# Performance work log

Hardware: AMD Instinct MI355X
Metric: run time of the kernel (lower is better)

The kernel has to match this reference:

```python
import jax, jax.numpy as jnp
import numpy as np

B, S, D, H = 2, 2048, 1024, 16
DK = D // H


def setup_inputs() -> dict:
    key = jax.random.key(0)
    ks = jax.random.split(key, 12)
    q = jax.random.normal(ks[0], (B, S, D), dtype=jnp.float32)
    k = jax.random.normal(ks[1], (B, S, D), dtype=jnp.float32)
    v = jax.random.normal(ks[2], (B, S, D), dtype=jnp.float32)
    # causal mask: 1 = attend, 0 = masked (masked_fill(mask==0, -inf))
    mask = jnp.tril(jnp.ones((S, S), dtype=jnp.int32))[None, None]
    w = 0.02
    Wq = jax.random.normal(ks[3], (D, D), dtype=jnp.float32) * w
    bq = jnp.zeros((D,), dtype=jnp.float32)
    Wk = jax.random.normal(ks[4], (D, D), dtype=jnp.float32) * w
    bk = jnp.zeros((D,), dtype=jnp.float32)
    Wv = jax.random.normal(ks[5], (D, D), dtype=jnp.float32) * w
    bv = jnp.zeros((D,), dtype=jnp.float32)
    Wo = jax.random.normal(ks[6], (D, D), dtype=jnp.float32) * w
    bo = jnp.zeros((D,), dtype=jnp.float32)
    return {"q": q, "k": k, "v": v, "mask": mask,
            "Wq": Wq, "bq": bq, "Wk": Wk, "bk": bk,
            "Wv": Wv, "bv": bv, "Wo": Wo, "bo": bo}


def _split_heads(x):
    b, s, _ = x.shape
    return x.reshape(b, s, H, DK).transpose(0, 2, 1, 3)  # [B,H,S,DK]


def reference(q, k, v, mask, Wq, bq, Wk, bk, Wv, bv, Wo, bo):
    qh = _split_heads(q @ Wq.T + bq)
    kh = _split_heads(k @ Wk.T + bk)
    vh = _split_heads(v @ Wv.T + bv)
    scale = 1.0 / jnp.sqrt(jnp.float32(DK))
    scores = jnp.einsum("bhqd,bhkd->bhqk", qh, kh) * scale  # [B,H,S,S]
    scores = jnp.where(mask == 0, -jnp.inf, scores)
    pesos = jax.nn.softmax(scores, axis=-1)
    pesos = jnp.nan_to_num(pesos, nan=0.0)  # fully-masked rows -> 0
    out = jnp.einsum("bhqk,bhkd->bhqd", pesos, vh)
    out = out.transpose(0, 2, 1, 3).reshape(q.shape[0], q.shape[1], D)
    # dropout is identity at inference
    return out @ Wo.T + bo
```

## Files before the change

kernel.cpp:

```cpp
#include <hip/hip_runtime.h>
#include <hip/hip_bf16.h>

#define B_  2
#define S_  2048
#define D_  1024
#define H_  16
#define DK_ 64

using bf16 = __hip_bfloat16;
typedef __bf16 bf16x8 __attribute__((ext_vector_type(8)));
typedef float  f32x4  __attribute__((ext_vector_type(4)));

__device__ inline void st1(float* p, float v) { *p = v; }
__device__ inline void st1(bf16*  p, float v) { *p = __float2bfloat16(v); }

__device__ inline void gll16(const bf16* g, bf16* l) {
    __builtin_amdgcn_global_load_lds(
        (const __attribute__((address_space(1))) unsigned int*)g,
        (__attribute__((address_space(3))) unsigned int*)l, 16, 0, 0);
}

__global__ __launch_bounds__(256) void cvt_kernel(
    const float* __restrict__ s0, const float* __restrict__ s1,
    const float* __restrict__ s2, const float* __restrict__ s3,
    const float* __restrict__ s4, const float* __restrict__ s5,
    const float* __restrict__ s6,
    bf16* __restrict__ d0, bf16* __restrict__ d1, bf16* __restrict__ d2,
    bf16* __restrict__ d3, bf16* __restrict__ d4, bf16* __restrict__ d5,
    bf16* __restrict__ d6, int nbig, int nsmall)
{
    const int z = blockIdx.y;
    const float* s; bf16* d; int n;
    switch (z) {
        case 0: s = s0; d = d0; n = nbig;   break;
        case 1: s = s1; d = d1; n = nbig;   break;
        case 2: s = s2; d = d2; n = nbig;   break;
        case 3: s = s3; d = d3; n = nsmall; break;
        case 4: s = s4; d = d4; n = nsmall; break;
        case 5: s = s5; d = d5; n = nsmall; break;
        default: s = s6; d = d6; n = nsmall; break;
    }
    const int idx = (blockIdx.x * 256 + threadIdx.x) * 4;
    if (idx < n) {
        const float4 v = *reinterpret_cast<const float4*>(s + idx);
        union { ushort4 u; __bf16 h[4]; } r;
        r.h[0] = (__bf16)v.x; r.h[1] = (__bf16)v.y;
        r.h[2] = (__bf16)v.z; r.h[3] = (__bf16)v.w;
        *reinterpret_cast<ushort4*>(d + idx) = r.u;
    }
}

template <typename TC, bool VT3, int BM>
__global__ __launch_bounds__(256, BM == 128 ? 3 : 4) void gemm_bt_kernel(
    const bf16* __restrict__ A0, const bf16* __restrict__ A1, const bf16* __restrict__ A2,
    const bf16* __restrict__ W0, const bf16* __restrict__ W1, const bf16* __restrict__ W2,
    const float* __restrict__ b0, const float* __restrict__ b1, const float* __restrict__ b2,
    TC* __restrict__ C0, TC* __restrict__ C1, TC* __restrict__ C2,
    int M, int N, int K)
{
    const int z = blockIdx.z;
    const bf16*  A    = (z == 0) ? A0 : (z == 1) ? A1 : A2;
    const bf16*  W    = (z == 0) ? W0 : (z == 1) ? W1 : W2;
    const float* bias = (z == 0) ? b0 : (z == 1) ? b1 : b2;
    TC*          C    = (z == 0) ? C0 : (z == 1) ? C1 : C2;

    __shared__ bf16 As[BM][32];
    __shared__ bf16 Bs[128][32];

    const int t    = threadIdx.x;
    const int lane = t & 63;
    const int wave = t >> 6;
    const int quad = lane >> 4;
    const int l16  = lane & 15;
    const int wm   = wave >> 1;
    const int wn   = wave & 1;

    const int m0 = blockIdx.y * BM;
    const int n0 = blockIdx.x * 128;

    constexpr int RPW = BM / 4;
    constexpr int MI  = BM / 32;
    const int ar0 = wave * RPW + (lane >> 2);
    const int br0 = wave * 32  + (lane >> 2);
    const int c0  = (lane & 3) * 8;
    const bf16* Ab = A + (size_t)(m0 + ar0) * K + c0;
    const bf16* Bb = W + (size_t)(n0 + br0) * K + c0;
    bf16* asd = &As[wave * RPW][0];
    bf16* bsd = &Bs[wave * 32][0];

    f32x4 acc[MI][4] = {};

    for (int kt = 0; kt < K; kt += 32) {
        __syncthreads();
        gll16(Ab + kt, asd);
        if constexpr (BM == 128) gll16(Ab + 16 * K + kt, asd + 16 * 32);
        gll16(Bb + kt, bsd);
        gll16(Bb + 16 * K + kt, bsd + 16 * 32);
        __syncthreads();

        bf16x8 af[MI], bfr[4];
#pragma unroll
        for (int mi = 0; mi < MI; mi++)
            af[mi] = *reinterpret_cast<const bf16x8*>(&As[wm * (BM / 2) + mi * 16 + l16][quad * 8]);
#pragma unroll
        for (int ni = 0; ni < 4; ni++)
            bfr[ni] = *reinterpret_cast<const bf16x8*>(&Bs[wn * 64 + ni * 16 + l16][quad * 8]);
#pragma unroll
        for (int mi = 0; mi < MI; mi++)
#pragma unroll
            for (int ni = 0; ni < 4; ni++)
                acc[mi][ni] = __builtin_amdgcn_mfma_f32_16x16x32_bf16(
                    af[mi], bfr[ni], acc[mi][ni], 0, 0, 0);
    }

    if (VT3 && z == 2) {
#pragma unroll
        for (int ni = 0; ni < 4; ni++) {
            const int col = n0 + wn * 64 + ni * 16 + l16;
            const float bvv = bias[col];
            const int hh = col >> 6, dh = col & 63;
#pragma unroll
            for (int mi = 0; mi < MI; mi++) {
                const int rb  = m0 + wm * (BM / 2) + mi * 16 + quad * 4;
                const int bb  = rb >> 11;
                const int tok = rb & (S_ - 1);
                union { ushort4 u; __bf16 h[4]; } pk;
#pragma unroll
                for (int i = 0; i < 4; i++)
                    pk.h[i] = (__bf16)(acc[mi][ni][i] + bvv);
                bf16* vt = (bf16*)C + ((size_t)(bb * H_ + hh) * DK_ + dh) * S_ + tok;
                *reinterpret_cast<ushort4*>(vt) = pk.u;
            }
        }
    } else {
#pragma unroll
        for (int ni = 0; ni < 4; ni++) {
            const int col = n0 + wn * 64 + ni * 16 + l16;
            const float bvv = bias[col];
#pragma unroll
            for (int mi = 0; mi < MI; mi++) {
#pragma unroll
                for (int i = 0; i < 4; i++) {
                    const int row = m0 + wm * (BM / 2) + mi * 16 + quad * 4 + i;
                    st1(&C[(size_t)row * N + col], acc[mi][ni][i] + bvv);
                }
            }
        }
    }
}

__global__ __launch_bounds__(256, 3) void attn_kernel(
    const bf16* __restrict__ Qp, const bf16* __restrict__ Kp,
    const bf16* __restrict__ VT, bf16* __restrict__ AO)
{
    const int t    = threadIdx.x;
    const int lane = t & 63;
    const int wave = t >> 6;
    const int quad = lane >> 4;
    const int l16  = lane & 15;

    const int til = 31 - blockIdx.x;
    const int h = blockIdx.y;
    const int b = blockIdx.z;
    const size_t bh = (size_t)b * S_ * D_ + (size_t)h * DK_;
    const bf16* vtb = VT + (size_t)(b * H_ + h) * DK_ * S_;

    __shared__ bf16 Ks[2][64][64];
    __shared__ bf16 Vs[2][64][64];
    __shared__ bf16 Pb[4][16][72];

    const int sR = lane >> 3;
    const int scg = ((lane & 7) ^ sR) * 8;
    const int swz0 = (quad ^ (l16 & 7)) * 8;
    const int swz1 = ((quad + 4) ^ (l16 & 7)) * 8;

    const float QSC = 0.18033688f;
    const float NEG = -1e30f;

    bf16x8 onesf;
#pragma unroll
    for (int j = 0; j < 8; j++) onesf[j] = (__bf16)1.0f;

    bf16x8 qf0, qf1;
    {
        const bf16* qrow = Qp + bh + (size_t)(til * 64 + wave * 16 + l16) * D_;
        qf0 = *reinterpret_cast<const bf16x8*>(qrow + quad * 8);
        qf1 = *reinterpret_cast<const bf16x8*>(qrow + 32 + quad * 8);
#pragma unroll
        for (int j = 0; j < 8; j++) {
            qf0[j] = (__bf16)((float)qf0[j] * QSC);
            qf1[j] = (__bf16)((float)qf1[j] * QSC);
        }
    }

    f32x4 lacc = {};
    f32x4 oacc[4] = {};

    const int ntot = til + 1;

    {
#pragma unroll
        for (int j = 0; j < 2; j++) {
            const int R = wave * 16 + j * 8 + sR;
            gll16(Kp + bh + (size_t)R * D_ + scg, &Ks[0][wave * 16 + j * 8][0]);
            gll16(vtb + (size_t)R * S_ + scg,     &Vs[0][wave * 16 + j * 8][0]);
        }
    }

    for (int it = 0; it < ntot; it++) {
        __syncthreads();

        if (it + 1 < ntot) {
            const int k0n = (it + 1) * 64;
            const int bufn = (it + 1) & 1;
#pragma unroll
            for (int j = 0; j < 2; j++) {
                const int R = wave * 16 + j * 8 + sR;
                gll16(Kp + bh + (size_t)(k0n + R) * D_ + scg, &Ks[bufn][wave * 16 + j * 8][0]);
                gll16(vtb + (size_t)R * S_ + k0n + scg,       &Vs[bufn][wave * 16 + j * 8][0]);
            }
        }

        const int k0  = it * 64;
        const int buf = it & 1;
        const int qw0 = til * 64 + wave * 16;

        f32x4 sc[4];
#pragma unroll
        for (int ch = 0; ch < 4; ch++) {
            const int row = ch * 16 + l16;
            bf16x8 kfa = *reinterpret_cast<const bf16x8*>(&Ks[buf][row][swz0]);
            bf16x8 kfb = *reinterpret_cast<const bf16x8*>(&Ks[buf][row][swz1]);
            f32x4 zz = {};
            zz = __builtin_amdgcn_mfma_f32_16x16x32_bf16(qf0, kfa, zz, 0, 0, 0);
            sc[ch] = __builtin_amdgcn_mfma_f32_16x16x32_bf16(qf1, kfb, zz, 0, 0, 0);
        }

        const bool bnd = (it == til);
#pragma unroll
        for (int i = 0; i < 4; i++) {
            const int r = quad * 4 + i;
            float s0 = sc[0][i], s1 = sc[1][i], s2 = sc[2][i], s3 = sc[3][i];
            if (bnd) {
                const int qi = qw0 + r;
                s0 = (k0 + l16      <= qi) ? s0 : NEG;
                s1 = (k0 + 16 + l16 <= qi) ? s1 : NEG;
                s2 = (k0 + 32 + l16 <= qi) ? s2 : NEG;
                s3 = (k0 + 48 + l16 <= qi) ? s3 : NEG;
            }
            Pb[wave][r][l16]      = __float2bfloat16(__builtin_amdgcn_exp2f(s0));
            Pb[wave][r][16 + l16] = __float2bfloat16(__builtin_amdgcn_exp2f(s1));
            Pb[wave][r][32 + l16] = __float2bfloat16(__builtin_amdgcn_exp2f(s2));
            Pb[wave][r][48 + l16] = __float2bfloat16(__builtin_amdgcn_exp2f(s3));
        }
        asm volatile("s_waitcnt lgkmcnt(0)" ::: "memory");
        bf16x8 pf0 = *reinterpret_cast<const bf16x8*>(&Pb[wave][l16][quad * 8]);
        bf16x8 pf1 = *reinterpret_cast<const bf16x8*>(&Pb[wave][l16][32 + quad * 8]);

        lacc = __builtin_amdgcn_mfma_f32_16x16x32_bf16(pf0, onesf, lacc, 0, 0, 0);
        lacc = __builtin_amdgcn_mfma_f32_16x16x32_bf16(pf1, onesf, lacc, 0, 0, 0);

#pragma unroll
        for (int n = 0; n < 4; n++) {
            const int row = n * 16 + l16;
            bf16x8 vt0 = *reinterpret_cast<const bf16x8*>(&Vs[buf][row][swz0]);
            bf16x8 vt1 = *reinterpret_cast<const bf16x8*>(&Vs[buf][row][swz1]);
            oacc[n] = __builtin_amdgcn_mfma_f32_16x16x32_bf16(pf0, vt0, oacc[n], 0, 0, 0);
            oacc[n] = __builtin_amdgcn_mfma_f32_16x16x32_bf16(pf1, vt1, oacc[n], 0, 0, 0);
        }
    }

    {
        const int qw0 = til * 64 + wave * 16;
#pragma unroll
        for (int i = 0; i < 4; i++) {
            const float inv = 1.0f / lacc[i];
#pragma unroll
            for (int n = 0; n < 4; n++)
                AO[bh + (size_t)(qw0 + quad * 4 + i) * D_ + n * 16 + l16] =
                    __float2bfloat16(oacc[n][i] * inv);
        }
    }
}

extern "C" void kernel_launch(void* const* d_in, const int* in_sizes, int n_in,
                              void* d_out, int out_size, void* d_ws, size_t ws_size,
                              hipStream_t stream)
{
    const float* q  = (const float*)d_in[0];
    const float* k  = (const float*)d_in[1];
    const float* v  = (const float*)d_in[2];
    const float* Wq = (const float*)d_in[4];
    const float* bq = (const float*)d_in[5];
    const float* Wk = (const float*)d_in[6];
    const float* bk = (const float*)d_in[7];
    const float* Wv = (const float*)d_in[8];
    const float* bv = (const float*)d_in[9];
    const float* Wo = (const float*)d_in[10];
    const float* bo = (const float*)d_in[11];
    float* out = (float*)d_out;

    bf16* ws = (bf16*)d_ws;
    const size_t MD = (size_t)(B_ * S_) * D_;
    const size_t WN = (size_t)D_ * D_;
    bf16* qb  = ws;
    bf16* kb  = ws + MD;
    bf16* vb  = ws + 2 * MD;
    bf16* wqb = ws + 3 * MD;
    bf16* wkb = wqb + WN;
    bf16* wvb = wkb + WN;
    bf16* wob = wvb + WN;
    bf16* Qp  = wob + WN;
    bf16* Kp  = Qp + MD;
    bf16* VT  = Kp + MD;
    bf16* AO  = Qp;

    const int M = B_ * S_;

    cvt_kernel<<<dim3((int)(MD / 4 / 256), 7), 256, 0, stream>>>(
        q, k, v, Wq, Wk, Wv, Wo, qb, kb, vb, wqb, wkb, wvb, wob,
        (int)MD, (int)WN);

    gemm_bt_kernel<bf16, true, 128><<<dim3(D_ / 128, M / 128, 3), 256, 0, stream>>>(
        qb, kb, vb, wqb, wkb, wvb, bq, bk, bv, Qp, Kp, VT, M, D_, D_);

    attn_kernel<<<dim3(32, H_, B_), 256, 0, stream>>>(Qp, Kp, VT, AO);

    gemm_bt_kernel<float, false, 64><<<dim3(D_ / 128, M / 64, 1), 256, 0, stream>>>(
        AO, AO, AO, wob, wob, wob, bo, bo, bo, out, out, out, M, D_, D_);
}
```

Before: 258.3 us.

## Pair long and short causal query tiles per block with 512-thread attention blocks

Attention blocks now cover 128 query rows with 8 waves. Each block handles one long causal tile and then one short one (15-i and i), so every block does the same 34 K/V chunk iterations. The change targets the load imbalance and tail effect of causal tiles, where late tiles did far more work than early ones. It also halves the K/V loads per query row, because one staged chunk now serves 128 rows. In exchange there are only 256 blocks with about 8 waves per CU. Waves past the diagonal sit idle through the barrier iterations, and an extra branch plus a mid-loop output write is added.

```diff
diff --git a/kernel.cpp b/kernel.cpp
--- a/kernel.cpp
+++ b/kernel.cpp
@@ -149,7 +149,7 @@
     }
 }
 
-__global__ __launch_bounds__(256, 3) void attn_kernel(
+__global__ __launch_bounds__(512, 4) void attn_kernel(
     const bf16* __restrict__ Qp, const bf16* __restrict__ Kp,
     const bf16* __restrict__ VT, bf16* __restrict__ AO)
 {
@@ -159,7 +159,9 @@
     const int quad = lane >> 4;
     const int l16  = lane & 15;
 
-    const int til = 31 - blockIdx.x;
+    const int pairi  = blockIdx.x;
+    const int TL     = 15 - pairi;
+    const int TS     = pairi;
     const int h = blockIdx.y;
     const int b = blockIdx.z;
     const size_t bh = (size_t)b * S_ * D_ + (size_t)h * DK_;
@@ -167,9 +169,9 @@
 
     __shared__ bf16 Ks[2][64][64];
     __shared__ bf16 Vs[2][64][64];
-    __shared__ bf16 Pb[4][16][72];
-
-    const int sR = lane >> 3;
+    __shared__ bf16 Pb[8][16][72];
+
+    const int sR  = lane >> 3;
     const int scg = ((lane & 7) ^ sR) * 8;
     const int swz0 = (quad ^ (l16 & 7)) * 8;
     const int swz1 = ((quad + 4) ^ (l16 & 7)) * 8;
@@ -181,9 +183,10 @@
 #pragma unroll
     for (int j = 0; j < 8; j++) onesf[j] = (__bf16)1.0f;
 
+    int til = TL;
     bf16x8 qf0, qf1;
     {
-        const bf16* qrow = Qp + bh + (size_t)(til * 64 + wave * 16 + l16) * D_;
+        const bf16* qrow = Qp + bh + (size_t)(til * 128 + wave * 16 + l16) * D_;
         qf0 = *reinterpret_cast<const bf16x8*>(qrow + quad * 8);
         qf1 = *reinterpret_cast<const bf16x8*>(qrow + 32 + quad * 8);
 #pragma unroll
@@ -196,34 +199,58 @@
     f32x4 lacc = {};
     f32x4 oacc[4] = {};
 
-    const int ntot = til + 1;
+    const int nA   = 2 * TL + 2;
+    const int ntot = 34;
 
     {
-#pragma unroll
-        for (int j = 0; j < 2; j++) {
-            const int R = wave * 16 + j * 8 + sR;
-            gll16(Kp + bh + (size_t)R * D_ + scg, &Ks[0][wave * 16 + j * 8][0]);
-            gll16(vtb + (size_t)R * S_ + scg,     &Vs[0][wave * 16 + j * 8][0]);
-        }
-    }
-
+        const int R = wave * 8 + sR;
+        gll16(Kp + bh + (size_t)R * D_ + scg, &Ks[0][wave * 8][0]);
+        gll16(vtb + (size_t)R * S_ + scg,     &Vs[0][wave * 8][0]);
+    }
+
+    int kcbase = 0;
     for (int it = 0; it < ntot; it++) {
         __syncthreads();
 
         if (it + 1 < ntot) {
-            const int k0n = (it + 1) * 64;
-            const int bufn = (it + 1) & 1;
-#pragma unroll
-            for (int j = 0; j < 2; j++) {
-                const int R = wave * 16 + j * 8 + sR;
-                gll16(Kp + bh + (size_t)(k0n + R) * D_ + scg, &Ks[bufn][wave * 16 + j * 8][0]);
-                gll16(vtb + (size_t)R * S_ + k0n + scg,       &Vs[bufn][wave * 16 + j * 8][0]);
-            }
-        }
-
-        const int k0  = it * 64;
+            const int itn  = it + 1;
+            const int k0n  = ((itn < nA) ? itn : itn - nA) * 64;
+            const int bufn = itn & 1;
+            const int R = wave * 8 + sR;
+            gll16(Kp + bh + (size_t)(k0n + R) * D_ + scg, &Ks[bufn][wave * 8][0]);
+            gll16(vtb + (size_t)R * S_ + k0n + scg,       &Vs[bufn][wave * 8][0]);
+        }
+
+        if (it == nA) {
+            const int qw0 = til * 128 + wave * 16;
+#pragma unroll
+            for (int i = 0; i < 4; i++) {
+                const float inv = 1.0f / lacc[i];
+#pragma unroll
+                for (int n = 0; n < 4; n++)
+                    AO[bh + (size_t)(qw0 + quad * 4 + i) * D_ + n * 16 + l16] =
+                        __float2bfloat16(oacc[n][i] * inv);
+            }
+            til = TS; kcbase = nA;
+            const bf16* qrow = Qp + bh + (size_t)(til * 128 + wave * 16 + l16) * D_;
+            qf0 = *reinterpret_cast<const bf16x8*>(qrow + quad * 8);
+            qf1 = *reinterpret_cast<const bf16x8*>(qrow + 32 + quad * 8);
+#pragma unroll
+            for (int j = 0; j < 8; j++) {
+                qf0[j] = (__bf16)((float)qf0[j] * QSC);
+                qf1[j] = (__bf16)((float)qf1[j] * QSC);
+            }
+            lacc = f32x4{};
+#pragma unroll
+            for (int n = 0; n < 4; n++) oacc[n] = f32x4{};
+        }
+
+        const int kc  = it - kcbase;
+        const int k0  = kc * 64;
         const int buf = it & 1;
-        const int qw0 = til * 64 + wave * 16;
+        const int qw0 = til * 128 + wave * 16;
+
+        if (k0 > qw0 + 15) continue;
 
         f32x4 sc[4];
 #pragma unroll
@@ -236,7 +263,7 @@
             sc[ch] = __builtin_amdgcn_mfma_f32_16x16x32_bf16(qf1, kfb, zz, 0, 0, 0);
         }
 
-        const bool bnd = (it == til);
+        const bool bnd = (k0 + 63 > qw0);
 #pragma unroll
         for (int i = 0; i < 4; i++) {
             const int r = quad * 4 + i;
@@ -271,7 +298,7 @@
     }
 
     {
-        const int qw0 = til * 64 + wave * 16;
+        const int qw0 = til * 128 + wave * 16;
 #pragma unroll
         for (int i = 0; i < 4; i++) {
             const float inv = 1.0f / lacc[i];
@@ -324,7 +351,7 @@
     gemm_bt_kernel<bf16, true, 128><<<dim3(D_ / 128, M / 128, 3), 256, 0, stream>>>(
         qb, kb, vb, wqb, wkb, wvb, bq, bk, bv, Qp, Kp, VT, M, D_, D_);
 
-    attn_kernel<<<dim3(32, H_, B_), 256, 0, stream>>>(Qp, Kp, VT, AO);
+    attn_kernel<<<dim3(8, H_, B_), 512, 0, stream>>>(Qp, Kp, VT, AO);
 
     gemm_bt_kernel<float, false, 64><<<dim3(D_ / 128, M / 64, 1), 256, 0, stream>>>(
         AO, AO, AO, wob, wob, wob, bo, bo, bo, out, out, out, M, D_, D_);
```

Result: faster. 237.6 us (-8.0%).

## Pair long and short causal query tiles per block with triple-buffered K/V

Applied to the files above, without the earlier changes.

Each attention block now processes two query tiles (31-i and i) sequentially, so every block does the same 33 key-tile iterations and the causal workload is balanced. The grid halves, and the K/V pipeline moves to three LDS buffers with explicit vmcnt waits and a single barrier per iteration. Occupancy hint drops to 2 blocks per CU because LDS use grows, which may reduce latency hiding.

```diff
diff --git a/kernel.cpp b/kernel.cpp
--- a/kernel.cpp
+++ b/kernel.cpp
@@ -149,7 +149,7 @@
     }
 }
 
-__global__ __launch_bounds__(256, 3) void attn_kernel(
+__global__ __launch_bounds__(256, 2) void attn_kernel(
     const bf16* __restrict__ Qp, const bf16* __restrict__ Kp,
     const bf16* __restrict__ VT, bf16* __restrict__ AO)
 {
@@ -159,14 +159,16 @@
     const int quad = lane >> 4;
     const int l16  = lane & 15;
 
-    const int til = 31 - blockIdx.x;
+    const int pairi  = blockIdx.x;
+    const int tLong  = 31 - pairi;
+    const int tShort = pairi;
     const int h = blockIdx.y;
     const int b = blockIdx.z;
     const size_t bh = (size_t)b * S_ * D_ + (size_t)h * DK_;
     const bf16* vtb = VT + (size_t)(b * H_ + h) * DK_ * S_;
 
-    __shared__ bf16 Ks[2][64][64];
-    __shared__ bf16 Vs[2][64][64];
+    __shared__ bf16 Ks[3][64][64];
+    __shared__ bf16 Vs[3][64][64];
     __shared__ bf16 Pb[4][16][72];
 
     const int sR = lane >> 3;
@@ -181,22 +183,31 @@
 #pragma unroll
     for (int j = 0; j < 8; j++) onesf[j] = (__bf16)1.0f;
 
-    bf16x8 qf0, qf1;
+    bf16x8 qA0, qA1, qB0, qB1;
     {
-        const bf16* qrow = Qp + bh + (size_t)(til * 64 + wave * 16 + l16) * D_;
-        qf0 = *reinterpret_cast<const bf16x8*>(qrow + quad * 8);
-        qf1 = *reinterpret_cast<const bf16x8*>(qrow + 32 + quad * 8);
+        const bf16* qrow = Qp + bh + (size_t)(tLong * 64 + wave * 16 + l16) * D_;
+        qA0 = *reinterpret_cast<const bf16x8*>(qrow + quad * 8);
+        qA1 = *reinterpret_cast<const bf16x8*>(qrow + 32 + quad * 8);
+        const bf16* qrs = Qp + bh + (size_t)(tShort * 64 + wave * 16 + l16) * D_;
+        qB0 = *reinterpret_cast<const bf16x8*>(qrs + quad * 8);
+        qB1 = *reinterpret_cast<const bf16x8*>(qrs + 32 + quad * 8);
 #pragma unroll
         for (int j = 0; j < 8; j++) {
-            qf0[j] = (__bf16)((float)qf0[j] * QSC);
-            qf1[j] = (__bf16)((float)qf1[j] * QSC);
-        }
-    }
+            qA0[j] = (__bf16)((float)qA0[j] * QSC);
+            qA1[j] = (__bf16)((float)qA1[j] * QSC);
+            qB0[j] = (__bf16)((float)qB0[j] * QSC);
+            qB1[j] = (__bf16)((float)qB1[j] * QSC);
+        }
+    }
+
+    int til = tLong;
+    bf16x8 qf0 = qA0, qf1 = qA1;
 
     f32x4 lacc = {};
     f32x4 oacc[4] = {};
 
-    const int ntot = til + 1;
+    const int nA   = tLong + 1;
+    const int ntot = 33;
 
     {
 #pragma unroll
@@ -207,36 +218,59 @@
         }
     }
 
+    int cur = 0, kcbase = 0;
     for (int it = 0; it < ntot; it++) {
-        __syncthreads();
+        const int nxt = (cur == 2) ? 0 : cur + 1;
 
         if (it + 1 < ntot) {
-            const int k0n = (it + 1) * 64;
-            const int bufn = (it + 1) & 1;
+            const int itn = it + 1;
+            const int k0n = ((itn < nA) ? itn : itn - nA) * 64;
 #pragma unroll
             for (int j = 0; j < 2; j++) {
                 const int R = wave * 16 + j * 8 + sR;
-                gll16(Kp + bh + (size_t)(k0n + R) * D_ + scg, &Ks[bufn][wave * 16 + j * 8][0]);
-                gll16(vtb + (size_t)R * S_ + k0n + scg,       &Vs[bufn][wave * 16 + j * 8][0]);
-            }
-        }
-
-        const int k0  = it * 64;
-        const int buf = it & 1;
+                gll16(Kp + bh + (size_t)(k0n + R) * D_ + scg, &Ks[nxt][wave * 16 + j * 8][0]);
+                gll16(vtb + (size_t)R * S_ + k0n + scg,       &Vs[nxt][wave * 16 + j * 8][0]);
+            }
+            asm volatile("s_waitcnt vmcnt(4)" ::: "memory");
+        } else {
+            asm volatile("s_waitcnt vmcnt(0)" ::: "memory");
+        }
+        __builtin_amdgcn_s_barrier();
+        asm volatile("" ::: "memory");
+
+        if (it == nA) {
+            const int qw0 = til * 64 + wave * 16;
+#pragma unroll
+            for (int i = 0; i < 4; i++) {
+                const float inv = 1.0f / lacc[i];
+#pragma unroll
+                for (int n = 0; n < 4; n++)
+                    AO[bh + (size_t)(qw0 + quad * 4 + i) * D_ + n * 16 + l16] =
+                        __float2bfloat16(oacc[n][i] * inv);
+            }
+            til = tShort; kcbase = nA;
+            qf0 = qB0; qf1 = qB1;
+            lacc = f32x4{};
+#pragma unroll
+            for (int n = 0; n < 4; n++) oacc[n] = f32x4{};
+        }
+
+        const int kc  = it - kcbase;
+        const int k0  = kc * 64;
         const int qw0 = til * 64 + wave * 16;
 
         f32x4 sc[4];
 #pragma unroll
         for (int ch = 0; ch < 4; ch++) {
             const int row = ch * 16 + l16;
-            bf16x8 kfa = *reinterpret_cast<const bf16x8*>(&Ks[buf][row][swz0]);
-            bf16x8 kfb = *reinterpret_cast<const bf16x8*>(&Ks[buf][row][swz1]);
+            bf16x8 kfa = *reinterpret_cast<const bf16x8*>(&Ks[cur][row][swz0]);
+            bf16x8 kfb = *reinterpret_cast<const bf16x8*>(&Ks[cur][row][swz1]);
             f32x4 zz = {};
             zz = __builtin_amdgcn_mfma_f32_16x16x32_bf16(qf0, kfa, zz, 0, 0, 0);
             sc[ch] = __builtin_amdgcn_mfma_f32_16x16x32_bf16(qf1, kfb, zz, 0, 0, 0);
         }
 
-        const bool bnd = (it == til);
+        const bool bnd = (kc == til);
 #pragma unroll
         for (int i = 0; i < 4; i++) {
             const int r = quad * 4 + i;
@@ -263,11 +297,13 @@
 #pragma unroll
         for (int n = 0; n < 4; n++) {
             const int row = n * 16 + l16;
-            bf16x8 vt0 = *reinterpret_cast<const bf16x8*>(&Vs[buf][row][swz0]);
-            bf16x8 vt1 = *reinterpret_cast<const bf16x8*>(&Vs[buf][row][swz1]);
+            bf16x8 vt0 = *reinterpret_cast<const bf16x8*>(&Vs[cur][row][swz0]);
+            bf16x8 vt1 = *reinterpret_cast<const bf16x8*>(&Vs[cur][row][swz1]);
             oacc[n] = __builtin_amdgcn_mfma_f32_16x16x32_bf16(pf0, vt0, oacc[n], 0, 0, 0);
             oacc[n] = __builtin_amdgcn_mfma_f32_16x16x32_bf16(pf1, vt1, oacc[n], 0, 0, 0);
         }
+
+        cur = nxt;
     }
 
     {
@@ -324,7 +360,7 @@
     gemm_bt_kernel<bf16, true, 128><<<dim3(D_ / 128, M / 128, 3), 256, 0, stream>>>(
         qb, kb, vb, wqb, wkb, wvb, bq, bk, bv, Qp, Kp, VT, M, D_, D_);
 
-    attn_kernel<<<dim3(32, H_, B_), 256, 0, stream>>>(Qp, Kp, VT, AO);
+    attn_kernel<<<dim3(16, H_, B_), 256, 0, stream>>>(Qp, Kp, VT, AO);
 
     gemm_bt_kernel<float, false, 64><<<dim3(D_ / 128, M / 64, 1), 256, 0, stream>>>(
         AO, AO, AO, wob, wob, wob, bo, bo, bo, out, out, out, M, D_, D_);
```

Result: faster. 228.5 us (-11.5%).

## Rework causal attention with 32x32 MFMA, paired tiles, and register P transpose

Applied to the files above, without the earlier changes.

The attention kernel moves to 128-row query tiles computed with 32x32x16 bf16 MFMAs. Each block handles one long and one short causal tile so every block does the same 34 key steps, which balances causal work. K and V move to a 4-deep LDS ring with explicit vmcnt waits. The P matrix is packed and transposed in registers with cvt_pk and permlane32_swap instead of going through an LDS round-trip. The grid drops to 256 blocks with one block per CU and no longer relies on occupancy to hide latency, so more depends on the software pipeline.

```diff
diff --git a/kernel.cpp b/kernel.cpp
--- a/kernel.cpp
+++ b/kernel.cpp
@@ -10,6 +10,7 @@
 using bf16 = __hip_bfloat16;
 typedef __bf16 bf16x8 __attribute__((ext_vector_type(8)));
 typedef float  f32x4  __attribute__((ext_vector_type(4)));
+typedef float  f32x16 __attribute__((ext_vector_type(16)));
 
 __device__ inline void st1(float* p, float v) { *p = v; }
 __device__ inline void st1(bf16*  p, float v) { *p = __float2bfloat16(v); }
@@ -18,6 +19,20 @@
     __builtin_amdgcn_global_load_lds(
         (const __attribute__((address_space(1))) unsigned int*)g,
         (__attribute__((address_space(3))) unsigned int*)l, 16, 0, 0);
+}
+
+__device__ inline f32x16 mfma32(bf16x8 a, bf16x8 b, f32x16 c) {
+    return __builtin_amdgcn_mfma_f32_32x32x16_bf16(a, b, c, 0, 0, 0);
+}
+
+__device__ inline unsigned cvtpk(float lo, float hi) {
+    unsigned r;
+    asm("v_cvt_pk_bf16_f32 %0, %1, %2" : "=v"(r) : "v"(lo), "v"(hi));
+    return r;
+}
+
+__device__ inline void plswap(unsigned &d, unsigned &s) {
+    asm volatile("v_permlane32_swap_b32 %0, %1" : "+v"(d), "+v"(s));
 }
 
 __global__ __launch_bounds__(256) void cvt_kernel(
@@ -149,136 +164,179 @@
     }
 }
 
-__global__ __launch_bounds__(256, 3) void attn_kernel(
+__global__ __launch_bounds__(256, 1) void attn_kernel(
     const bf16* __restrict__ Qp, const bf16* __restrict__ Kp,
     const bf16* __restrict__ VT, bf16* __restrict__ AO)
 {
     const int t    = threadIdx.x;
     const int lane = t & 63;
     const int wave = t >> 6;
-    const int quad = lane >> 4;
-    const int l16  = lane & 15;
-
-    const int til = 31 - blockIdx.x;
+    const int r31  = lane & 31;
+    const int hl   = lane >> 5;
+    const int l7   = lane & 7;
+
+    const int pairi = blockIdx.x;
+    const int TL    = 15 - pairi;
+    const int TS    = pairi;
     const int h = blockIdx.y;
     const int b = blockIdx.z;
     const size_t bh = (size_t)b * S_ * D_ + (size_t)h * DK_;
     const bf16* vtb = VT + (size_t)(b * H_ + h) * DK_ * S_;
 
-    __shared__ bf16 Ks[2][64][64];
-    __shared__ bf16 Vs[2][64][64];
-    __shared__ bf16 Pb[4][16][72];
-
-    const int sR = lane >> 3;
+    __shared__ bf16 Ks[4][64][64];
+    __shared__ bf16 Vs[4][64][64];
+
+    const int sR  = lane >> 3;
     const int scg = ((lane & 7) ^ sR) * 8;
-    const int swz0 = (quad ^ (l16 & 7)) * 8;
-    const int swz1 = ((quad + 4) ^ (l16 & 7)) * 8;
 
     const float QSC = 0.18033688f;
     const float NEG = -1e30f;
 
-    bf16x8 onesf;
-#pragma unroll
-    for (int j = 0; j < 8; j++) onesf[j] = (__bf16)1.0f;
-
-    bf16x8 qf0, qf1;
+    bf16x8 ONES;
+#pragma unroll
+    for (int j = 0; j < 8; j++) ONES[j] = (__bf16)1.0f;
+
+    const int nA   = 2 * TL + 2;
+    const int ntot = 34;
+
+    int til = TL;
+    bf16x8 qf[4];
     {
-        const bf16* qrow = Qp + bh + (size_t)(til * 64 + wave * 16 + l16) * D_;
-        qf0 = *reinterpret_cast<const bf16x8*>(qrow + quad * 8);
-        qf1 = *reinterpret_cast<const bf16x8*>(qrow + 32 + quad * 8);
-#pragma unroll
-        for (int j = 0; j < 8; j++) {
-            qf0[j] = (__bf16)((float)qf0[j] * QSC);
-            qf1[j] = (__bf16)((float)qf1[j] * QSC);
-        }
-    }
-
-    f32x4 lacc = {};
-    f32x4 oacc[4] = {};
-
-    const int ntot = til + 1;
+        const bf16* qr = Qp + bh + (size_t)(TL * 128 + wave * 32 + r31) * D_ + 8 * hl;
+#pragma unroll
+        for (int d = 0; d < 4; d++) {
+            qf[d] = *reinterpret_cast<const bf16x8*>(qr + 16 * d);
+#pragma unroll
+            for (int j = 0; j < 8; j++) qf[d][j] = (__bf16)((float)qf[d][j] * QSC);
+        }
+    }
+
+    f32x16 oacc0 = {}, oacc1 = {}, lacc = {};
+
+    auto stage = [&](int slot) {
+        const int k0n = ((slot < nA) ? slot : slot - nA) * 64;
+        const int bb  = slot & 3;
+#pragma unroll
+        for (int j = 0; j < 2; j++) {
+            const int rb = wave * 16 + j * 8;
+            gll16(Kp + bh + (size_t)(k0n + rb + sR) * D_ + scg, &Ks[bb][rb][0]);
+            gll16(vtb + (size_t)(rb + sR) * S_ + k0n + scg,     &Vs[bb][rb][0]);
+        }
+    };
+
+    stage(0);
+    stage(1);
+
+    int kcbase = 0;
+    for (int it = 0; it < ntot; it++) {
+        if (it + 2 < ntot) {
+            stage(it + 2);
+            asm volatile("s_waitcnt vmcnt(8)" ::: "memory");
+        } else if (it + 1 < ntot) {
+            asm volatile("s_waitcnt vmcnt(4)" ::: "memory");
+        } else {
+            asm volatile("s_waitcnt vmcnt(0)" ::: "memory");
+        }
+        __builtin_amdgcn_s_barrier();
+
+        if (it == nA) {
+            const int qb0 = til * 128 + wave * 32;
+#pragma unroll
+            for (int r = 0; r < 16; r++) {
+                const int q = qb0 + (r & 3) + 8 * (r >> 2) + 4 * hl;
+                const float inv = 1.0f / lacc[r];
+                AO[bh + (size_t)q * D_ + r31]      = __float2bfloat16(oacc0[r] * inv);
+                AO[bh + (size_t)q * D_ + 32 + r31] = __float2bfloat16(oacc1[r] * inv);
+            }
+            til = TS; kcbase = nA;
+            const bf16* qr = Qp + bh + (size_t)(TS * 128 + wave * 32 + r31) * D_ + 8 * hl;
+#pragma unroll
+            for (int d = 0; d < 4; d++) {
+                qf[d] = *reinterpret_cast<const bf16x8*>(qr + 16 * d);
+#pragma unroll
+                for (int j = 0; j < 8; j++) qf[d][j] = (__bf16)((float)qf[d][j] * QSC);
+            }
+            oacc0 = f32x16{}; oacc1 = f32x16{}; lacc = f32x16{};
+        }
+
+        const int kc  = it - kcbase;
+        const int k0  = kc * 64;
+        const int buf = it & 3;
+        const int qw0 = til * 128 + wave * 32;
+
+        if (k0 <= qw0 + 31) {
+            f32x16 s0 = {}, s1 = {};
+#pragma unroll
+            for (int d = 0; d < 4; d++) {
+                const int g = ((2 * d + hl) ^ l7) * 8;
+                const bf16x8 kf0 = *reinterpret_cast<const bf16x8*>(&Ks[buf][r31][g]);
+                const bf16x8 kf1 = *reinterpret_cast<const bf16x8*>(&Ks[buf][32 + r31][g]);
+                s0 = mfma32(kf0, qf[d], s0);
+                s1 = mfma32(kf1, qf[d], s1);
+            }
+
+            if (k0 + 63 > qw0) {
+                const int qg = qw0 + r31;
+                const int kb = k0 + 4 * hl;
+#pragma unroll
+                for (int r = 0; r < 16; r++) {
+                    const int ko = (r & 3) + 8 * (r >> 2);
+                    s0[r] = (kb + ko      <= qg) ? s0[r] : NEG;
+                    s1[r] = (kb + 32 + ko <= qg) ? s1[r] : NEG;
+                }
+            }
+
+#pragma unroll
+            for (int r = 0; r < 16; r++) {
+                s0[r] = __builtin_amdgcn_exp2f(s0[r]);
+                s1[r] = __builtin_amdgcn_exp2f(s1[r]);
+            }
+
+            bf16x8 pa[4];
+#pragma unroll
+            for (int G = 0; G < 2; G++) {
+#pragma unroll
+                for (int tt = 0; tt < 2; tt++) {
+                    unsigned a01, a23, a45, a67;
+                    if (G == 0) {
+                        a01 = cvtpk(s0[8*tt+0], s0[8*tt+1]);
+                        a23 = cvtpk(s0[8*tt+2], s0[8*tt+3]);
+                        a45 = cvtpk(s0[8*tt+4], s0[8*tt+5]);
+                        a67 = cvtpk(s0[8*tt+6], s0[8*tt+7]);
+                    } else {
+                        a01 = cvtpk(s1[8*tt+0], s1[8*tt+1]);
+                        a23 = cvtpk(s1[8*tt+2], s1[8*tt+3]);
+                        a45 = cvtpk(s1[8*tt+4], s1[8*tt+5]);
+                        a67 = cvtpk(s1[8*tt+6], s1[8*tt+7]);
+                    }
+                    plswap(a01, a45);
+                    plswap(a23, a67);
+                    union { unsigned u[4]; bf16x8 v; } pu;
+                    pu.u[0] = a01; pu.u[1] = a23; pu.u[2] = a45; pu.u[3] = a67;
+                    pa[2 * G + tt] = pu.v;
+                }
+            }
+
+#pragma unroll
+            for (int s = 0; s < 4; s++) {
+                const int g = ((2 * s + hl) ^ l7) * 8;
+                const bf16x8 vf0 = *reinterpret_cast<const bf16x8*>(&Vs[buf][r31][g]);
+                const bf16x8 vf1 = *reinterpret_cast<const bf16x8*>(&Vs[buf][32 + r31][g]);
+                oacc0 = mfma32(pa[s], vf0, oacc0);
+                oacc1 = mfma32(pa[s], vf1, oacc1);
+                lacc  = mfma32(pa[s], ONES, lacc);
+            }
+        }
+    }
 
     {
-#pragma unroll
-        for (int j = 0; j < 2; j++) {
-            const int R = wave * 16 + j * 8 + sR;
-            gll16(Kp + bh + (size_t)R * D_ + scg, &Ks[0][wave * 16 + j * 8][0]);
-            gll16(vtb + (size_t)R * S_ + scg,     &Vs[0][wave * 16 + j * 8][0]);
-        }
-    }
-
-    for (int it = 0; it < ntot; it++) {
-        __syncthreads();
-
-        if (it + 1 < ntot) {
-            const int k0n = (it + 1) * 64;
-            const int bufn = (it + 1) & 1;
-#pragma unroll
-            for (int j = 0; j < 2; j++) {
-                const int R = wave * 16 + j * 8 + sR;
-                gll16(Kp + bh + (size_t)(k0n + R) * D_ + scg, &Ks[bufn][wave * 16 + j * 8][0]);
-                gll16(vtb + (size_t)R * S_ + k0n + scg,       &Vs[bufn][wave * 16 + j * 8][0]);
-            }
-        }
-
-        const int k0  = it * 64;
-        const int buf = it & 1;
-        const int qw0 = til * 64 + wave * 16;
-
-        f32x4 sc[4];
-#pragma unroll
-        for (int ch = 0; ch < 4; ch++) {
-            const int row = ch * 16 + l16;
-            bf16x8 kfa = *reinterpret_cast<const bf16x8*>(&Ks[buf][row][swz0]);
-            bf16x8 kfb = *reinterpret_cast<const bf16x8*>(&Ks[buf][row][swz1]);
-            f32x4 zz = {};
-            zz = __builtin_amdgcn_mfma_f32_16x16x32_bf16(qf0, kfa, zz, 0, 0, 0);
-            sc[ch] = __builtin_amdgcn_mfma_f32_16x16x32_bf16(qf1, kfb, zz, 0, 0, 0);
-        }
-
-        const bool bnd = (it == til);
-#pragma unroll
-        for (int i = 0; i < 4; i++) {
-            const int r = quad * 4 + i;
-            float s0 = sc[0][i], s1 = sc[1][i], s2 = sc[2][i], s3 = sc[3][i];
-            if (bnd) {
-                const int qi = qw0 + r;
-                s0 = (k0 + l16      <= qi) ? s0 : NEG;
-                s1 = (k0 + 16 + l16 <= qi) ? s1 : NEG;
-                s2 = (k0 + 32 + l16 <= qi) ? s2 : NEG;
-                s3 = (k0 + 48 + l16 <= qi) ? s3 : NEG;
-            }
-            Pb[wave][r][l16]      = __float2bfloat16(__builtin_amdgcn_exp2f(s0));
-            Pb[wave][r][16 + l16] = __float2bfloat16(__builtin_amdgcn_exp2f(s1));
-            Pb[wave][r][32 + l16] = __float2bfloat16(__builtin_amdgcn_exp2f(s2));
-            Pb[wave][r][48 + l16] = __float2bfloat16(__builtin_amdgcn_exp2f(s3));
-        }
-        asm volatile("s_waitcnt lgkmcnt(0)" ::: "memory");
-        bf16x8 pf0 = *reinterpret_cast<const bf16x8*>(&Pb[wave][l16][quad * 8]);
-        bf16x8 pf1 = *reinterpret_cast<const bf16x8*>(&Pb[wave][l16][32 + quad * 8]);
-
-        lacc = __builtin_amdgcn_mfma_f32_16x16x32_bf16(pf0, onesf, lacc, 0, 0, 0);
-        lacc = __builtin_amdgcn_mfma_f32_16x16x32_bf16(pf1, onesf, lacc, 0, 0, 0);
-
-#pragma unroll
-        for (int n = 0; n < 4; n++) {
-            const int row = n * 16 + l16;
-            bf16x8 vt0 = *reinterpret_cast<const bf16x8*>(&Vs[buf][row][swz0]);
-            bf16x8 vt1 = *reinterpret_cast<const bf16x8*>(&Vs[buf][row][swz1]);
-            oacc[n] = __builtin_amdgcn_mfma_f32_16x16x32_bf16(pf0, vt0, oacc[n], 0, 0, 0);
-            oacc[n] = __builtin_amdgcn_mfma_f32_16x16x32_bf16(pf1, vt1, oacc[n], 0, 0, 0);
-        }
-    }
-
-    {
-        const int qw0 = til * 64 + wave * 16;
-#pragma unroll
-        for (int i = 0; i < 4; i++) {
-            const float inv = 1.0f / lacc[i];
-#pragma unroll
-            for (int n = 0; n < 4; n++)
-                AO[bh + (size_t)(qw0 + quad * 4 + i) * D_ + n * 16 + l16] =
-                    __float2bfloat16(oacc[n][i] * inv);
+        const int qb0 = til * 128 + wave * 32;
+#pragma unroll
+        for (int r = 0; r < 16; r++) {
+            const int q = qb0 + (r & 3) + 8 * (r >> 2) + 4 * hl;
+            const float inv = 1.0f / lacc[r];
+            AO[bh + (size_t)q * D_ + r31]      = __float2bfloat16(oacc0[r] * inv);
+            AO[bh + (size_t)q * D_ + 32 + r31] = __float2bfloat16(oacc1[r] * inv);
         }
     }
 }
@@ -324,7 +382,7 @@
     gemm_bt_kernel<bf16, true, 128><<<dim3(D_ / 128, M / 128, 3), 256, 0, stream>>>(
         qb, kb, vb, wqb, wkb, wvb, bq, bk, bv, Qp, Kp, VT, M, D_, D_);
 
-    attn_kernel<<<dim3(32, H_, B_), 256, 0, stream>>>(Qp, Kp, VT, AO);
+    attn_kernel<<<dim3(8, H_, B_), 256, 0, stream>>>(Qp, Kp, VT, AO);
 
     gemm_bt_kernel<float, false, 64><<<dim3(D_ / 128, M / 64, 1), 256, 0, stream>>>(
         AO, AO, AO, wob, wob, wob, bo, bo, bo, out, out, out, M, D_, D_);
```

New measurement: 241.8 us. -6.4%, faster.
